# Performance work log

Hardware: AMD Instinct MI355X
Metric: run time of the kernel (lower is better)

Reference implementation:

```python
import jax, jax.numpy as jnp
import numpy as np

B, S = 4096, 4096
NS, FDIM = 16, 64


def _ln(x, g, b):
    mu = jnp.mean(x, axis=-1, keepdims=True)
    v = jnp.mean((x - mu) ** 2, axis=-1, keepdims=True)
    return (x - mu) / jnp.sqrt(v + 1e-5) * g + b


def _rolling_vol_mean(returns, w):
    # mean over all length-w windows of unbiased std (matches per-window torch.std loop)
    Bn, L = returns.shape
    z = jnp.zeros((Bn, 1), returns.dtype)
    c1 = jnp.concatenate([z, jnp.cumsum(returns, axis=1)], axis=1)
    c2 = jnp.concatenate([z, jnp.cumsum(returns * returns, axis=1)], axis=1)
    s = c1[:, w:] - c1[:, :-w]    # [B, L-w+1] window sums
    s2 = c2[:, w:] - c2[:, :-w]
    var = (s2 - s * s / w) / (w - 1)
    return jnp.mean(jnp.sqrt(jnp.maximum(var, 0.0)), axis=1, keepdims=True)


def setup_inputs() -> dict:
    key = jax.random.key(0)
    ks = jax.random.split(key, 24)
    r = lambda i, shp: jax.random.normal(ks[i], shp, jnp.float32) * 0.05
    return {
        'price_series': jax.random.uniform(ks[0], (B, S, 1), jnp.float32) * 10.0 + 1.0,
        're_W': r(1, (4, 4, 64)), 're_b': r(2, (4, 64)),
        're_g': jnp.ones((4, 64), jnp.float32), 're_beta': jnp.zeros((4, 64), jnp.float32),
        'rh_W1': r(3, (256, 64)), 'rh_b1': r(4, (64,)), 'rh_W2': r(5, (64, 4)), 'rh_b2': r(6, (4,)),
        'rv_W': r(7, (3, 128)), 'rv_b': r(8, (128,)),
        'rv_g': jnp.ones((128,), jnp.float32), 'rv_beta': jnp.zeros((128,), jnp.float32),
        'vs_W': r(9, (128, 128)), 'vs_b': r(10, (128,)),
        'vs_g': jnp.ones((128,), jnp.float32), 'vs_beta': jnp.zeros((128,), jnp.float32),
        'vc_W1': r(11, (256, 64)), 'vc_b1': r(12, (64,)), 'vc_W2': r(13, (64, 4)), 'vc_b2': r(14, (4,)),
        'emb': r(15, (NS, FDIM)),
        'cn_W1': r(16, (576, 128)), 'cn_b1': r(17, (128,)),
        'cn_W2': r(18, (128, 64)), 'cn_b2': r(19, (64,)),
        'cn_W3': r(20, (64, 1)), 'cn_b3': r(21, (1,)),
    }


def reference(price_series, re_W, re_b, re_g, re_beta, rh_W1, rh_b1, rh_W2, rh_b2,
              rv_W, rv_b, rv_g, rv_beta, vs_W, vs_b, vs_g, vs_beta,
              vc_W1, vc_b1, vc_W2, vc_b2, emb, cn_W1, cn_b1, cn_W2, cn_b2, cn_W3, cn_b3):
    prices = price_series[:, :, 0]            # [B,S]
    Bn, Sn = prices.shape
    # --- MarketRegimeEncoder: SMA-20 via prefix sums (the per-step torch loop) ---
    cs = jnp.cumsum(prices, axis=1)
    shifted = jnp.concatenate([jnp.zeros((Bn, 20), prices.dtype), cs[:, :-20]], axis=1)
    counts = jnp.minimum(jnp.arange(Sn) + 1, 20).astype(prices.dtype)
    sma20 = (cs - shifted) / counts           # (sma_5 is computed but unused in original)
    trend = jnp.mean((prices - sma20) / (sma20 + 1e-8), axis=1, keepdims=True)
    p10 = prices[:, Sn - 10:Sn - 9]
    momentum = (prices[:, -1:] - p10) / (p10 + 1e-8)
    pmean = jnp.mean(prices, axis=1, keepdims=True)
    mean_rev = (prices[:, -1:] - pmean) / (pmean + 1e-8)
    pstd = jnp.std(prices, axis=1, keepdims=True, ddof=1)
    cycle = pstd / (pmean + 1e-8)
    combined = jnp.concatenate([trend, momentum, mean_rev, cycle], axis=1)  # [B,4]
    h = jax.nn.relu(jnp.einsum('bi,kio->bko', combined, re_W) + re_b[None])  # [B,4,64]
    h = _ln(h, re_g[None], re_beta[None])
    regime_features = h.reshape(Bn, -1)        # [B,256] (trend|momentum|mean_rev|cycle)
    logits = jax.nn.relu(regime_features @ rh_W1 + rh_b1) @ rh_W2 + rh_b2
    regime_probs = jax.nn.softmax(logits, axis=1)
    # --- VolatilityEncodingModule ---
    logp = jnp.log(jnp.maximum(price_series, 1e-8))
    returns = jnp.diff(logp, axis=1)[:, :, 0]  # [B,S-1]
    vol_in = jnp.concatenate([_rolling_vol_mean(returns, w) for w in (5, 10, 20)], axis=1)  # [B,3]
    rv = _ln(jax.nn.relu(vol_in @ rv_W + rv_b), rv_g, rv_beta)
    vs = _ln(jax.nn.relu(rv @ vs_W + vs_b), vs_g, vs_beta)
    vol_features = jnp.concatenate([rv, vs], axis=1)  # [B,256]
    vlogits = jax.nn.relu(vol_features @ vc_W1 + vc_b1) @ vc_W2 + vc_b2
    vol_regime = jax.nn.softmax(vlogits, axis=1)
    # --- OptionsStrategyEncoder: vectorized over strategies ---
    mv = jnp.concatenate([regime_features, vol_features], axis=1)  # [B,512]
    mvp = mv @ cn_W1[:512]                    # [B,128]
    ep = emb @ cn_W1[512:]                    # [NS,128]
    h1 = jax.nn.relu(mvp[:, None, :] + ep[None, :, :] + cn_b1)  # [B,NS,128]
    h2 = jax.nn.relu(h1 @ cn_W2 + cn_b2)      # [B,NS,64]
    scores = (h2 @ cn_W3 + cn_b3)[:, :, 0]    # [B,NS]
    return regime_features, regime_probs, vol_features, vol_regime, scores
```

## Files before the change

kernel.cpp:

```cpp
#include <hip/hip_runtime.h>
#include <math.h>

#define NROWS 4096
#define SLEN  4096
#define RETN  4095
#define CHK   20

__global__ __launch_bounds__(256) void k_ep(const float* __restrict__ emb,
                                            const float* __restrict__ cn_W1,
                                            const float* __restrict__ cn_b1,
                                            float* __restrict__ ep) {
    int idx = blockIdx.x * 256 + threadIdx.x;
    if (idx >= 16 * 128) return;
    int n = idx >> 7, o = idx & 127;
    float acc = cn_b1[o];
    const float* w = cn_W1 + 512 * 128;
    for (int i = 0; i < 64; ++i) acc = fmaf(emb[n * 64 + i], w[i * 128 + o], acc);
    ep[idx] = acc;
}

__global__ void k_stats(const float* __restrict__ price,
                        float* __restrict__ combined,
                        float* __restrict__ volin) {
    __shared__ float scm[260 * CHK];
    __shared__ float red[6][4];

    const int tid = threadIdx.x;
    const int row = blockIdx.x;
    const float* pr = price + (size_t)row * SLEN;

    float pA = 0.f, pB = 0.f;
    if (tid == 0) { pA = pr[SLEN - 10]; pB = pr[SLEN - 1]; }

    if (tid < 40) { scm[tid] = 0.f; scm[258 * CHK + tid] = 0.f; }

    #pragma unroll
    for (int it = 0; it < 4; ++it) {
        const int i = it * 256 + tid;
        const float4 v = ((const float4*)pr)[i];
        *(float4*)&scm[(2 + (i >> 2)) * CHK + ((4 * i) & 15)] = v;
    }
    __syncthreads();

    const int s0 = tid * 16;

    float hb[20], x_[16];
    *(float4*)&hb[0] = *(const float4*)&scm[tid * CHK + 12];
    #pragma unroll
    for (int k = 0; k < 4; ++k)
        *(float4*)&hb[4 + 4 * k] = *(const float4*)&scm[(tid + 1) * CHK + 4 * k];
    #pragma unroll
    for (int k = 0; k < 4; ++k)
        *(float4*)&x_[4 * k] = *(const float4*)&scm[(tid + 2) * CHK + 4 * k];
    const float pn = scm[(tid + 3) * CHK];

    float W = 0.f;
    #pragma unroll
    for (int k = 0; k < 20; ++k) W += hb[k];
    float st = 0.f, s1p = 0.f, s2p = 0.f;
    #pragma unroll
    for (int d = 0; d < 16; ++d) {
        const float x = x_[d];
        W += x - hb[d];
        float inv_cnt = 0.05f;
        if (s0 == 0)                 inv_cnt = 1.0f / (float)(d + 1);
        else if (s0 == 16 && d < 3)  inv_cnt = 1.0f / (float)(17 + d);
        const float sma = W * inv_cnt;
        st  = fmaf(x - sma, __builtin_amdgcn_rcpf(sma + 1e-8f), st);
        s1p += x;
        s2p = fmaf(x, x, s2p);
    }

    float lg[17];
    #pragma unroll
    for (int d = 0; d < 16; ++d) lg[d] = __builtin_amdgcn_logf(fmaxf(x_[d], 1e-8f));
    lg[16] = __builtin_amdgcn_logf(fmaxf(pn, 1e-8f));
    float rs[36];
    #pragma unroll
    for (int d = 0; d < 16; ++d) rs[d] = lg[d + 1] - lg[d];

    __syncthreads();
    #pragma unroll
    for (int k = 0; k < 4; ++k)
        *(float4*)&scm[(tid + 2) * CHK + 4 * k] = *(const float4*)&rs[4 * k];
    __syncthreads();

    #pragma unroll
    for (int k = 0; k < 4; ++k)
        *(float4*)&rs[16 + 4 * k] = *(const float4*)&scm[(tid + 3) * CHK + 4 * k];
    *(float4*)&rs[32] = *(const float4*)&scm[(tid + 4) * CHK];

    float S5 = 0.f, Q5 = 0.f, S10 = 0.f, Q10 = 0.f, S20 = 0.f, Q20 = 0.f;
    #pragma unroll
    for (int j = 0; j < 20; ++j) {
        const float x = rs[j];
        S20 += x; Q20 = fmaf(x, x, Q20);
        if (j < 10) { S10 += x; Q10 = fmaf(x, x, Q10); }
        if (j < 5)  { S5  += x; Q5  = fmaf(x, x, Q5); }
    }

    #define SQT(S, Q, invw) \
        __builtin_amdgcn_sqrtf(fmaxf(fmaf(-(S) * (invw), (S), (Q)), 0.f))

    float v5 = 0.f, v10 = 0.f, v20 = 0.f;
    if (tid < 254) {
        #pragma unroll
        for (int d = 0; d < 16; ++d) {
            v5  += SQT(S5,  Q5,  0.2f);
            v10 += SQT(S10, Q10, 0.1f);
            v20 += SQT(S20, Q20, 0.05f);
            const float xo = rs[d], qo = xo * xo;
            const float a5 = rs[d + 5], a10 = rs[d + 10], a20 = rs[d + 20];
            S5  += a5  - xo;  Q5  = fmaf(a5,  a5,  Q5)  - qo;
            S10 += a10 - xo;  Q10 = fmaf(a10, a10, Q10) - qo;
            S20 += a20 - xo;  Q20 = fmaf(a20, a20, Q20) - qo;
        }
    } else {
        #pragma unroll
        for (int d = 0; d < 16; ++d) {
            const int i = s0 + d;
            if (i < 4091) v5  += SQT(S5,  Q5,  0.2f);
            if (i < 4086) v10 += SQT(S10, Q10, 0.1f);
            if (i < 4076) v20 += SQT(S20, Q20, 0.05f);
            const float xo = rs[d], qo = xo * xo;
            const float a5 = rs[d + 5], a10 = rs[d + 10], a20 = rs[d + 20];
            S5  += a5  - xo;  Q5  = fmaf(a5,  a5,  Q5)  - qo;
            S10 += a10 - xo;  Q10 = fmaf(a10, a10, Q10) - qo;
            S20 += a20 - xo;  Q20 = fmaf(a20, a20, Q20) - qo;
        }
    }
    #undef SQT

    {
        float vals[6] = {s1p, s2p, st, v5, v10, v20};
        const int lane = tid & 63, wid = tid >> 6;
        #pragma unroll
        for (int v = 0; v < 6; ++v) {
            float x = vals[v];
            for (int o = 32; o > 0; o >>= 1) x += __shfl_xor(x, o, 64);
            if (lane == 0) red[v][wid] = x;
        }
    }
    __syncthreads();
    if (tid == 0) {
        const float sum_p  = red[0][0] + red[0][1] + red[0][2] + red[0][3];
        const float sum_p2 = red[1][0] + red[1][1] + red[1][2] + red[1][3];
        const float sum_t  = red[2][0] + red[2][1] + red[2][2] + red[2][3];
        const float sv5    = red[3][0] + red[3][1] + red[3][2] + red[3][3];
        const float sv10   = red[4][0] + red[4][1] + red[4][2] + red[4][3];
        const float sv20   = red[5][0] + red[5][1] + red[5][2] + red[5][3];
        const float pmean = sum_p * (1.f / 4096.f);
        const float varp  = fmaf(-sum_p * (1.f / 4096.f), sum_p, sum_p2) * (1.f / 4095.f);
        const float pstd  = __builtin_amdgcn_sqrtf(fmaxf(varp, 0.f));
        const float ipm   = __builtin_amdgcn_rcpf(pmean + 1e-8f);
        combined[row * 4 + 0] = sum_t * (1.f / 4096.f);
        combined[row * 4 + 1] = (pB - pA) * __builtin_amdgcn_rcpf(pA + 1e-8f);
        combined[row * 4 + 2] = (pB - pmean) * ipm;
        combined[row * 4 + 3] = pstd * ipm;
        const float LN2 = 0.6931471805599453f;
        volin[row * 3 + 0] = sv5  * (LN2 * 0.5f                 / 4091.f);
        volin[row * 3 + 1] = sv10 * (LN2 * (1.f / 3.f)          / 4086.f);
        volin[row * 3 + 2] = sv20 * (LN2 * 0.22941573387056174f / 4076.f);
    }
}

__global__ __launch_bounds__(512, 2) void k_mc(const float* __restrict__ combined,
                                               const float* __restrict__ volin,
                                               const float* __restrict__ re_W,  const float* __restrict__ re_b,
                                               const float* __restrict__ re_g,  const float* __restrict__ re_be,
                                               const float* __restrict__ rh_W1, const float* __restrict__ rh_b1,
                                               const float* __restrict__ rh_W2, const float* __restrict__ rh_b2,
                                               const float* __restrict__ rv_W,  const float* __restrict__ rv_b,
                                               const float* __restrict__ rv_g,  const float* __restrict__ rv_be,
                                               const float* __restrict__ vs_W,  const float* __restrict__ vs_b,
                                               const float* __restrict__ vs_g,  const float* __restrict__ vs_be,
                                               const float* __restrict__ vc_W1, const float* __restrict__ vc_b1,
                                               const float* __restrict__ vc_W2, const float* __restrict__ vc_b2,
                                               const float* __restrict__ cn_W1,
                                               const float* __restrict__ cn_W2,
                                               const float* __restrict__ cn_b2,
                                               const float* __restrict__ cn_W3,
                                               const float* __restrict__ cn_b3,
                                               const float* __restrict__ ep,
                                               float* __restrict__ out_rf, float* __restrict__ out_rp,
                                               float* __restrict__ out_vf, float* __restrict__ out_vr,
                                               float* __restrict__ scores) {
    __shared__ __align__(16) float w2s[128 * 64];
    __shared__ __align__(16) float epb[16][132];
    __shared__ __align__(16) float rf_lds[8][256];
    __shared__ __align__(16) float vf_lds[8][256];
    __shared__ __align__(16) float psx[4][8][128];
    __shared__ __align__(16) float mvp_s[8][132];
    __shared__ float hid_s[8][64];
    __shared__ float prt[8][4];
    __shared__ float cmb_s[8][4];
    __shared__ float vol_s[8][3];

    const int tid  = threadIdx.x;
    const int lane = tid & 63;
    const int wid  = tid >> 6;
    const int row0 = blockIdx.x * 8;

    #pragma unroll
    for (int k = 0; k < 4; ++k) {
        const int idx = k * 512 + tid;
        *(float4*)&w2s[4 * idx] = *(const float4*)(cn_W2 + 4 * idx);
    }
    {
        const int ns = tid >> 5, c4 = (tid & 31) * 4;
        *(float4*)&epb[ns][c4] = *(const float4*)(ep + ns * 128 + c4);
    }
    if (tid < 32) cmb_s[tid >> 2][tid & 3] = combined[(size_t)(row0 + (tid >> 2)) * 4 + (tid & 3)];
    else if (tid < 56) { int t = tid - 32; vol_s[t / 3][t % 3] = volin[(size_t)(row0 + t / 3) * 3 + t % 3]; }
    __syncthreads();

    const int role = wid & 3;
    const int rg   = (wid >> 2) * 4;

    {
        const float* w = re_W + role * 256;
        const float w0 = w[lane], w1 = w[64 + lane], w2 = w[128 + lane], w3 = w[192 + lane];
        const float b  = re_b[role * 64 + lane];
        const float gg = re_g[role * 64 + lane], bb = re_be[role * 64 + lane];
        float h[4], sm[4], sq[4];
        #pragma unroll
        for (int r = 0; r < 4; ++r) {
            const int rr = rg + r;
            float v = fmaf(cmb_s[rr][0], w0, fmaf(cmb_s[rr][1], w1,
                      fmaf(cmb_s[rr][2], w2, fmaf(cmb_s[rr][3], w3, b))));
            h[r] = fmaxf(v, 0.f);
            sm[r] = h[r]; sq[r] = h[r] * h[r];
        }
        #pragma unroll
        for (int off = 32; off > 0; off >>= 1) {
            #pragma unroll
            for (int r = 0; r < 4; ++r) {
                sm[r] += __shfl_xor(sm[r], off, 64);
                sq[r] += __shfl_xor(sq[r], off, 64);
            }
        }
        #pragma unroll
        for (int r = 0; r < 4; ++r) {
            const float mu  = sm[r] * (1.f / 64.f);
            const float var = fmaxf(sq[r] * (1.f / 64.f) - mu * mu, 0.f);
            const float y = (h[r] - mu) * rsqrtf(var + 1e-5f) * gg + bb;
            rf_lds[rg + r][role * 64 + lane] = y;
            out_rf[(size_t)(row0 + rg + r) * 256 + role * 64 + lane] = y;
        }
    }
    __syncthreads();

    {
        const int i0 = role * 64;
        float acc[4] = {0.f, 0.f, 0.f, 0.f};
        for (int i = 0; i < 64; ++i) {
            const float wv = rh_W1[(size_t)(i0 + i) * 64 + lane];
            #pragma unroll
            for (int r = 0; r < 4; ++r) acc[r] = fmaf(rf_lds[rg + r][i0 + i], wv, acc[r]);
        }
        #pragma unroll
        for (int r = 0; r < 4; ++r) psx[role][rg + r][lane] = acc[r];
    }
    __syncthreads();

    {
        const int r = tid >> 6, o = tid & 63;
        const float v = psx[0][r][o] + psx[1][r][o] + psx[2][r][o] + psx[3][r][o] + rh_b1[o];
        hid_s[r][o] = fmaxf(v, 0.f);
    }
    __syncthreads();

    if (tid < 32) {
        const int r = tid >> 2, j = tid & 3;
        float acc = rh_b2[j];
        for (int i = 0; i < 64; ++i) acc = fmaf(hid_s[r][i], rh_W2[i * 4 + j], acc);
        float m = acc;
        m = fmaxf(m, __shfl_xor(m, 1, 64));
        m = fmaxf(m, __shfl_xor(m, 2, 64));
        const float e = expf(acc - m);
        float s = e;
        s += __shfl_xor(s, 1, 64);
        s += __shfl_xor(s, 2, 64);
        out_rp[(size_t)(row0 + r) * 4 + j] = e / s;
    }

    {
        const int o = tid & 127, g = tid >> 7;
        const float w0 = rv_W[o], w1 = rv_W[128 + o], w2 = rv_W[256 + o];
        const float b = rv_b[o], gg = rv_g[o], bb = rv_be[o];
        float h[2], sm[2], sq[2];
        #pragma unroll
        for (int r2 = 0; r2 < 2; ++r2) {
            const int r = g * 2 + r2;
            float v = fmaf(vol_s[r][0], w0, fmaf(vol_s[r][1], w1, fmaf(vol_s[r][2], w2, b)));
            h[r2] = fmaxf(v, 0.f);
            sm[r2] = h[r2]; sq[r2] = h[r2] * h[r2];
        }
        #pragma unroll
        for (int off = 32; off > 0; off >>= 1) {
            #pragma unroll
            for (int r2 = 0; r2 < 2; ++r2) {
                sm[r2] += __shfl_xor(sm[r2], off, 64);
                sq[r2] += __shfl_xor(sq[r2], off, 64);
            }
        }
        if (lane == 0) {
            #pragma unroll
            for (int r2 = 0; r2 < 2; ++r2) { prt[wid][r2 * 2] = sm[r2]; prt[wid][r2 * 2 + 1] = sq[r2]; }
        }
        __syncthreads();
        #pragma unroll
        for (int r2 = 0; r2 < 2; ++r2) {
            const float S = prt[2 * g][2 * r2]     + prt[2 * g + 1][2 * r2];
            const float Q = prt[2 * g][2 * r2 + 1] + prt[2 * g + 1][2 * r2 + 1];
            const float mu  = S * (1.f / 128.f);
            const float var = fmaxf(Q * (1.f / 128.f) - mu * mu, 0.f);
            const float y = (h[r2] - mu) * rsqrtf(var + 1e-5f) * gg + bb;
            vf_lds[g * 2 + r2][o] = y;
            out_vf[(size_t)(row0 + g * 2 + r2) * 256 + o] = y;
        }
    }
    __syncthreads();

    {
        const int o = tid & 127, g = tid >> 7;
        float acc[2];
        const float b = vs_b[o];
        acc[0] = b; acc[1] = b;
        for (int i = 0; i < 128; ++i) {
            const float wv = vs_W[(size_t)i * 128 + o];
            #pragma unroll
            for (int r2 = 0; r2 < 2; ++r2) acc[r2] = fmaf(vf_lds[g * 2 + r2][i], wv, acc[r2]);
        }
        const float gg = vs_g[o], bb = vs_be[o];
        float h[2], sm[2], sq[2];
        #pragma unroll
        for (int r2 = 0; r2 < 2; ++r2) {
            h[r2] = fmaxf(acc[r2], 0.f);
            sm[r2] = h[r2]; sq[r2] = h[r2] * h[r2];
        }
        #pragma unroll
        for (int off = 32; off > 0; off >>= 1) {
            #pragma unroll
            for (int r2 = 0; r2 < 2; ++r2) {
                sm[r2] += __shfl_xor(sm[r2], off, 64);
                sq[r2] += __shfl_xor(sq[r2], off, 64);
            }
        }
        __syncthreads();
        if (lane == 0) {
            #pragma unroll
            for (int r2 = 0; r2 < 2; ++r2) { prt[wid][r2 * 2] = sm[r2]; prt[wid][r2 * 2 + 1] = sq[r2]; }
        }
        __syncthreads();
        #pragma unroll
        for (int r2 = 0; r2 < 2; ++r2) {
            const float S = prt[2 * g][2 * r2]     + prt[2 * g + 1][2 * r2];
            const float Q = prt[2 * g][2 * r2 + 1] + prt[2 * g + 1][2 * r2 + 1];
            const float mu  = S * (1.f / 128.f);
            const float var = fmaxf(Q * (1.f / 128.f) - mu * mu, 0.f);
            const float y = (h[r2] - mu) * rsqrtf(var + 1e-5f) * gg + bb;
            vf_lds[g * 2 + r2][128 + o] = y;
            out_vf[(size_t)(row0 + g * 2 + r2) * 256 + 128 + o] = y;
        }
    }
    __syncthreads();

    {
        const int i0 = role * 64;
        float acc[4] = {0.f, 0.f, 0.f, 0.f};
        for (int i = 0; i < 64; ++i) {
            const float wv = vc_W1[(size_t)(i0 + i) * 64 + lane];
            #pragma unroll
            for (int r = 0; r < 4; ++r) acc[r] = fmaf(vf_lds[rg + r][i0 + i], wv, acc[r]);
        }
        #pragma unroll
        for (int r = 0; r < 4; ++r) psx[role][rg + r][lane] = acc[r];
    }
    __syncthreads();

    {
        const int r = tid >> 6, o = tid & 63;
        const float v = psx[0][r][o] + psx[1][r][o] + psx[2][r][o] + psx[3][r][o] + vc_b1[o];
        hid_s[r][o] = fmaxf(v, 0.f);
    }
    __syncthreads();
    if (tid < 32) {
        const int r = tid >> 2, j = tid & 3;
        float acc = vc_b2[j];
        for (int i = 0; i < 64; ++i) acc = fmaf(hid_s[r][i], vc_W2[i * 4 + j], acc);
        float m = acc;
        m = fmaxf(m, __shfl_xor(m, 1, 64));
        m = fmaxf(m, __shfl_xor(m, 2, 64));
        const float e = expf(acc - m);
        float s = e;
        s += __shfl_xor(s, 1, 64);
        s += __shfl_xor(s, 2, 64);
        out_vr[(size_t)(row0 + r) * 4 + j] = e / s;
    }
    __syncthreads();

    {
        const int p = lane >> 5;
        const int q = lane & 31;
        const float* mbase = (role < 2) ? &rf_lds[0][0] + role * 128
                                        : &vf_lds[0][0] + (role - 2) * 128;
        float acc[4][4] = {{0.f}};
        #pragma unroll 8
        for (int s = 0; s < 64; ++s) {
            const int i = 2 * s + p;
            const float4 w1v = *(const float4*)(cn_W1 + (size_t)(role * 128 + i) * 128 + 4 * q);
            #pragma unroll
            for (int r = 0; r < 4; ++r) {
                const float m = mbase[(rg + r) * 256 + i];
                acc[r][0] = fmaf(m, w1v.x, acc[r][0]);
                acc[r][1] = fmaf(m, w1v.y, acc[r][1]);
                acc[r][2] = fmaf(m, w1v.z, acc[r][2]);
                acc[r][3] = fmaf(m, w1v.w, acc[r][3]);
            }
        }
        #pragma unroll
        for (int r = 0; r < 4; ++r) {
            #pragma unroll
            for (int k = 0; k < 4; ++k) acc[r][k] += __shfl_xor(acc[r][k], 32, 64);
        }
        if (p == 0) {
            #pragma unroll
            for (int r = 0; r < 4; ++r)
                *(float4*)&psx[role][rg + r][4 * q] =
                    make_float4(acc[r][0], acc[r][1], acc[r][2], acc[r][3]);
        }
    }
    __syncthreads();

    #pragma unroll
    for (int k = 0; k < 2; ++k) {
        const int idx = k * 512 + tid;
        const int r = idx >> 7, c = idx & 127;
        mvp_s[r][c] = psx[0][r][c] + psx[1][r][c] + psx[2][r][c] + psx[3][r][c];
    }
    __syncthreads();

    {
        const int rgB = tid >> 8;
        const int nst = tid & 255;
        const int ns  = nst >> 4;
        const int t   = nst & 15;
        float acc[4][4];
        #pragma unroll
        for (int r = 0; r < 4; ++r)
            #pragma unroll
            for (int k = 0; k < 4; ++k) acc[r][k] = 0.f;

        #pragma unroll 2
        for (int c = 0; c < 128; c += 4) {
            float4 m4[4];
            #pragma unroll
            for (int r = 0; r < 4; ++r) m4[r] = *(const float4*)&mvp_s[rgB * 4 + r][c];
            const float4 e4 = *(const float4*)&epb[ns][c];
            {   const float4 w2v = *(const float4*)&w2s[(c + 0) * 64 + 4 * t];
                #pragma unroll
                for (int r = 0; r < 4; ++r) {
                    const float h = fmaxf(m4[r].x + e4.x, 0.f);
                    acc[r][0] = fmaf(h, w2v.x, acc[r][0]); acc[r][1] = fmaf(h, w2v.y, acc[r][1]);
                    acc[r][2] = fmaf(h, w2v.z, acc[r][2]); acc[r][3] = fmaf(h, w2v.w, acc[r][3]); } }
            {   const float4 w2v = *(const float4*)&w2s[(c + 1) * 64 + 4 * t];
                #pragma unroll
                for (int r = 0; r < 4; ++r) {
                    const float h = fmaxf(m4[r].y + e4.y, 0.f);
                    acc[r][0] = fmaf(h, w2v.x, acc[r][0]); acc[r][1] = fmaf(h, w2v.y, acc[r][1]);
                    acc[r][2] = fmaf(h, w2v.z, acc[r][2]); acc[r][3] = fmaf(h, w2v.w, acc[r][3]); } }
            {   const float4 w2v = *(const float4*)&w2s[(c + 2) * 64 + 4 * t];
                #pragma unroll
                for (int r = 0; r < 4; ++r) {
                    const float h = fmaxf(m4[r].z + e4.z, 0.f);
                    acc[r][0] = fmaf(h, w2v.x, acc[r][0]); acc[r][1] = fmaf(h, w2v.y, acc[r][1]);
                    acc[r][2] = fmaf(h, w2v.z, acc[r][2]); acc[r][3] = fmaf(h, w2v.w, acc[r][3]); } }
            {   const float4 w2v = *(const float4*)&w2s[(c + 3) * 64 + 4 * t];
                #pragma unroll
                for (int r = 0; r < 4; ++r) {
                    const float h = fmaxf(m4[r].w + e4.w, 0.f);
                    acc[r][0] = fmaf(h, w2v.x, acc[r][0]); acc[r][1] = fmaf(h, w2v.y, acc[r][1]);
                    acc[r][2] = fmaf(h, w2v.z, acc[r][2]); acc[r][3] = fmaf(h, w2v.w, acc[r][3]); } }
        }

        const float4 b2v = *(const float4*)(cn_b2 + 4 * t);
        const float4 w3v = *(const float4*)(cn_W3 + 4 * t);
        const float  b3v = cn_b3[0];
        #pragma unroll
        for (int r = 0; r < 4; ++r) {
            float s =      fmaxf(acc[r][0] + b2v.x, 0.f) * w3v.x;
            s = fmaf(fmaxf(acc[r][1] + b2v.y, 0.f), w3v.y, s);
            s = fmaf(fmaxf(acc[r][2] + b2v.z, 0.f), w3v.z, s);
            s = fmaf(fmaxf(acc[r][3] + b2v.w, 0.f), w3v.w, s);
            s += __shfl_xor(s, 1, 64);
            s += __shfl_xor(s, 2, 64);
            s += __shfl_xor(s, 4, 64);
            s += __shfl_xor(s, 8, 64);
            if (t == 0) scores[(size_t)(row0 + rgB * 4 + r) * 16 + ns] = s + b3v;
        }
    }
}

extern "C" void kernel_launch(void* const* d_in, const int* in_sizes, int n_in,
                              void* d_out, int out_size, void* d_ws, size_t ws_size,
                              hipStream_t stream) {
    (void)in_sizes; (void)n_in; (void)out_size; (void)ws_size;

    const float* price = (const float*)d_in[0];
    const float* re_W  = (const float*)d_in[1];
    const float* re_b  = (const float*)d_in[2];
    const float* re_g  = (const float*)d_in[3];
    const float* re_be = (const float*)d_in[4];
    const float* rh_W1 = (const float*)d_in[5];
    const float* rh_b1 = (const float*)d_in[6];
    const float* rh_W2 = (const float*)d_in[7];
    const float* rh_b2 = (const float*)d_in[8];
    const float* rv_W  = (const float*)d_in[9];
    const float* rv_b  = (const float*)d_in[10];
    const float* rv_g  = (const float*)d_in[11];
    const float* rv_be = (const float*)d_in[12];
    const float* vs_W  = (const float*)d_in[13];
    const float* vs_b  = (const float*)d_in[14];
    const float* vs_g  = (const float*)d_in[15];
    const float* vs_be = (const float*)d_in[16];
    const float* vc_W1 = (const float*)d_in[17];
    const float* vc_b1 = (const float*)d_in[18];
    const float* vc_W2 = (const float*)d_in[19];
    const float* vc_b2 = (const float*)d_in[20];
    const float* emb   = (const float*)d_in[21];
    const float* cn_W1 = (const float*)d_in[22];
    const float* cn_b1 = (const float*)d_in[23];
    const float* cn_W2 = (const float*)d_in[24];
    const float* cn_b2 = (const float*)d_in[25];
    const float* cn_W3 = (const float*)d_in[26];
    const float* cn_b3 = (const float*)d_in[27];

    float* out    = (float*)d_out;
    float* out_rf = out;
    float* out_rp = out_rf + 4096 * 256;
    float* out_vf = out_rp + 4096 * 4;
    float* out_vr = out_vf + 4096 * 256;
    float* out_sc = out_vr + 4096 * 4;

    float* ws       = (float*)d_ws;
    float* combined = ws;
    float* volin    = combined + 4096 * 4;
    float* ep       = volin + 4096 * 3;

    hipLaunchKernelGGL(k_ep,    dim3(8),    dim3(256), 0, stream, emb, cn_W1, cn_b1, ep);
    hipLaunchKernelGGL(k_stats, dim3(4096), dim3(256), 0, stream, price, combined, volin);
    hipLaunchKernelGGL(k_mc,    dim3(512),  dim3(512), 0, stream, combined, volin,
                       re_W, re_b, re_g, re_be, rh_W1, rh_b1, rh_W2, rh_b2,
                       rv_W, rv_b, rv_g, rv_be, vs_W, vs_b, vs_g, vs_be,
                       vc_W1, vc_b1, vc_W2, vc_b2,
                       cn_W1, cn_W2, cn_b2, cn_W3, cn_b3, ep,
                       out_rf, out_rp, out_vf, out_vr, out_sc);
}
```

Measured before the change: 110.3 us.

## Halve k_mc block to 4 rows/256 threads and alias LDS scratch buffers

```diff
diff --git a/kernel.cpp b/kernel.cpp
--- a/kernel.cpp
+++ b/kernel.cpp
@@ -19,9 +19,9 @@
     ep[idx] = acc;
 }
 
-__global__ void k_stats(const float* __restrict__ price,
-                        float* __restrict__ combined,
-                        float* __restrict__ volin) {
+__global__ __launch_bounds__(256, 4) void k_stats(const float* __restrict__ price,
+                                                  float* __restrict__ combined,
+                                                  float* __restrict__ volin) {
     __shared__ float scm[260 * CHK];
     __shared__ float red[6][4];
 
@@ -164,7 +164,7 @@
     }
 }
 
-__global__ __launch_bounds__(512, 2) void k_mc(const float* __restrict__ combined,
+__global__ __launch_bounds__(256, 3) void k_mc(const float* __restrict__ combined,
                                                const float* __restrict__ volin,
                                                const float* __restrict__ re_W,  const float* __restrict__ re_b,
                                                const float* __restrict__ re_g,  const float* __restrict__ re_be,
@@ -186,48 +186,42 @@
                                                float* __restrict__ out_vf, float* __restrict__ out_vr,
                                                float* __restrict__ scores) {
     __shared__ __align__(16) float w2s[128 * 64];
-    __shared__ __align__(16) float epb[16][132];
-    __shared__ __align__(16) float rf_lds[8][256];
-    __shared__ __align__(16) float vf_lds[8][256];
-    __shared__ __align__(16) float psx[4][8][128];
-    __shared__ __align__(16) float mvp_s[8][132];
-    __shared__ float hid_s[8][64];
-    __shared__ float prt[8][4];
-    __shared__ float cmb_s[8][4];
-    __shared__ float vol_s[8][3];
+    __shared__ __align__(16) float uni[2112];
+    __shared__ __align__(16) float rf_lds[4][256];
+    __shared__ __align__(16) float vf_lds[4][256];
+    __shared__ __align__(16) float mvp_s[4][128];
+    __shared__ float hid_s[4][64];
+    __shared__ float prt[4][4];
+    __shared__ float cmb_s[4][4];
+    __shared__ float vol_s[4][3];
 
     const int tid  = threadIdx.x;
     const int lane = tid & 63;
     const int wid  = tid >> 6;
-    const int row0 = blockIdx.x * 8;
-
-    #pragma unroll
-    for (int k = 0; k < 4; ++k) {
-        const int idx = k * 512 + tid;
+    const int row0 = blockIdx.x * 4;
+
+    const float4 ep0 = ((const float4*)ep)[2 * tid];
+    const float4 ep1 = ((const float4*)ep)[2 * tid + 1];
+
+    #pragma unroll
+    for (int k = 0; k < 8; ++k) {
+        const int idx = k * 256 + tid;
         *(float4*)&w2s[4 * idx] = *(const float4*)(cn_W2 + 4 * idx);
     }
-    {
-        const int ns = tid >> 5, c4 = (tid & 31) * 4;
-        *(float4*)&epb[ns][c4] = *(const float4*)(ep + ns * 128 + c4);
-    }
-    if (tid < 32) cmb_s[tid >> 2][tid & 3] = combined[(size_t)(row0 + (tid >> 2)) * 4 + (tid & 3)];
-    else if (tid < 56) { int t = tid - 32; vol_s[t / 3][t % 3] = volin[(size_t)(row0 + t / 3) * 3 + t % 3]; }
-    __syncthreads();
-
-    const int role = wid & 3;
-    const int rg   = (wid >> 2) * 4;
-
-    {
-        const float* w = re_W + role * 256;
+    if (tid < 16) cmb_s[tid >> 2][tid & 3] = combined[(size_t)(row0 + (tid >> 2)) * 4 + (tid & 3)];
+    else if (tid < 28) { int t = tid - 16; vol_s[t / 3][t % 3] = volin[(size_t)(row0 + t / 3) * 3 + t % 3]; }
+    __syncthreads();
+
+    {
+        const float* w = re_W + wid * 256;
         const float w0 = w[lane], w1 = w[64 + lane], w2 = w[128 + lane], w3 = w[192 + lane];
-        const float b  = re_b[role * 64 + lane];
-        const float gg = re_g[role * 64 + lane], bb = re_be[role * 64 + lane];
+        const float b  = re_b[wid * 64 + lane];
+        const float gg = re_g[wid * 64 + lane], bb = re_be[wid * 64 + lane];
         float h[4], sm[4], sq[4];
         #pragma unroll
         for (int r = 0; r < 4; ++r) {
-            const int rr = rg + r;
-            float v = fmaf(cmb_s[rr][0], w0, fmaf(cmb_s[rr][1], w1,
-                      fmaf(cmb_s[rr][2], w2, fmaf(cmb_s[rr][3], w3, b))));
+            float v = fmaf(cmb_s[r][0], w0, fmaf(cmb_s[r][1], w1,
+                      fmaf(cmb_s[r][2], w2, fmaf(cmb_s[r][3], w3, b))));
             h[r] = fmaxf(v, 0.f);
             sm[r] = h[r]; sq[r] = h[r] * h[r];
         }
@@ -244,33 +238,34 @@
             const float mu  = sm[r] * (1.f / 64.f);
             const float var = fmaxf(sq[r] * (1.f / 64.f) - mu * mu, 0.f);
             const float y = (h[r] - mu) * rsqrtf(var + 1e-5f) * gg + bb;
-            rf_lds[rg + r][role * 64 + lane] = y;
-            out_rf[(size_t)(row0 + rg + r) * 256 + role * 64 + lane] = y;
-        }
-    }
-    __syncthreads();
-
-    {
-        const int i0 = role * 64;
+            rf_lds[r][wid * 64 + lane] = y;
+            out_rf[(size_t)(row0 + r) * 256 + wid * 64 + lane] = y;
+        }
+    }
+    __syncthreads();
+
+    {
+        const int i0 = wid * 64;
         float acc[4] = {0.f, 0.f, 0.f, 0.f};
         for (int i = 0; i < 64; ++i) {
             const float wv = rh_W1[(size_t)(i0 + i) * 64 + lane];
             #pragma unroll
-            for (int r = 0; r < 4; ++r) acc[r] = fmaf(rf_lds[rg + r][i0 + i], wv, acc[r]);
-        }
-        #pragma unroll
-        for (int r = 0; r < 4; ++r) psx[role][rg + r][lane] = acc[r];
+            for (int r = 0; r < 4; ++r) acc[r] = fmaf(rf_lds[r][i0 + i], wv, acc[r]);
+        }
+        #pragma unroll
+        for (int r = 0; r < 4; ++r) uni[wid * 512 + r * 128 + lane] = acc[r];
     }
     __syncthreads();
 
     {
         const int r = tid >> 6, o = tid & 63;
-        const float v = psx[0][r][o] + psx[1][r][o] + psx[2][r][o] + psx[3][r][o] + rh_b1[o];
+        const float v = uni[r * 128 + o] + uni[512 + r * 128 + o]
+                      + uni[1024 + r * 128 + o] + uni[1536 + r * 128 + o] + rh_b1[o];
         hid_s[r][o] = fmaxf(v, 0.f);
     }
     __syncthreads();
 
-    if (tid < 32) {
+    if (tid < 16) {
         const int r = tid >> 2, j = tid & 3;
         float acc = rh_b2[j];
         for (int i = 0; i < 64; ++i) acc = fmaf(hid_s[r][i], rh_W2[i * 4 + j], acc);
@@ -367,25 +362,26 @@
     __syncthreads();
 
     {
-        const int i0 = role * 64;
+        const int i0 = wid * 64;
         float acc[4] = {0.f, 0.f, 0.f, 0.f};
         for (int i = 0; i < 64; ++i) {
             const float wv = vc_W1[(size_t)(i0 + i) * 64 + lane];
             #pragma unroll
-            for (int r = 0; r < 4; ++r) acc[r] = fmaf(vf_lds[rg + r][i0 + i], wv, acc[r]);
-        }
-        #pragma unroll
-        for (int r = 0; r < 4; ++r) psx[role][rg + r][lane] = acc[r];
+            for (int r = 0; r < 4; ++r) acc[r] = fmaf(vf_lds[r][i0 + i], wv, acc[r]);
+        }
+        #pragma unroll
+        for (int r = 0; r < 4; ++r) uni[wid * 512 + r * 128 + lane] = acc[r];
     }
     __syncthreads();
 
     {
         const int r = tid >> 6, o = tid & 63;
-        const float v = psx[0][r][o] + psx[1][r][o] + psx[2][r][o] + psx[3][r][o] + vc_b1[o];
+        const float v = uni[r * 128 + o] + uni[512 + r * 128 + o]
+                      + uni[1024 + r * 128 + o] + uni[1536 + r * 128 + o] + vc_b1[o];
         hid_s[r][o] = fmaxf(v, 0.f);
     }
     __syncthreads();
-    if (tid < 32) {
+    if (tid < 16) {
         const int r = tid >> 2, j = tid & 3;
         float acc = vc_b2[j];
         for (int i = 0; i < 64; ++i) acc = fmaf(hid_s[r][i], vc_W2[i * 4 + j], acc);
@@ -403,16 +399,16 @@
     {
         const int p = lane >> 5;
         const int q = lane & 31;
-        const float* mbase = (role < 2) ? &rf_lds[0][0] + role * 128
-                                        : &vf_lds[0][0] + (role - 2) * 128;
+        const float* mbase = (wid < 2) ? &rf_lds[0][0] + wid * 128
+                                       : &vf_lds[0][0] + (wid - 2) * 128;
         float acc[4][4] = {{0.f}};
         #pragma unroll 8
         for (int s = 0; s < 64; ++s) {
             const int i = 2 * s + p;
-            const float4 w1v = *(const float4*)(cn_W1 + (size_t)(role * 128 + i) * 128 + 4 * q);
+            const float4 w1v = *(const float4*)(cn_W1 + (size_t)(wid * 128 + i) * 128 + 4 * q);
             #pragma unroll
             for (int r = 0; r < 4; ++r) {
-                const float m = mbase[(rg + r) * 256 + i];
+                const float m = mbase[r * 256 + i];
                 acc[r][0] = fmaf(m, w1v.x, acc[r][0]);
                 acc[r][1] = fmaf(m, w1v.y, acc[r][1]);
                 acc[r][2] = fmaf(m, w1v.z, acc[r][2]);
@@ -427,7 +423,7 @@
         if (p == 0) {
             #pragma unroll
             for (int r = 0; r < 4; ++r)
-                *(float4*)&psx[role][rg + r][4 * q] =
+                *(float4*)&uni[wid * 512 + r * 128 + 4 * q] =
                     make_float4(acc[r][0], acc[r][1], acc[r][2], acc[r][3]);
         }
     }
@@ -435,17 +431,23 @@
 
     #pragma unroll
     for (int k = 0; k < 2; ++k) {
-        const int idx = k * 512 + tid;
+        const int idx = k * 256 + tid;
         const int r = idx >> 7, c = idx & 127;
-        mvp_s[r][c] = psx[0][r][c] + psx[1][r][c] + psx[2][r][c] + psx[3][r][c];
-    }
-    __syncthreads();
-
-    {
-        const int rgB = tid >> 8;
-        const int nst = tid & 255;
-        const int ns  = nst >> 4;
-        const int t   = nst & 15;
+        mvp_s[r][c] = uni[r * 128 + c] + uni[512 + r * 128 + c]
+                    + uni[1024 + r * 128 + c] + uni[1536 + r * 128 + c];
+    }
+    __syncthreads();
+
+    {
+        const int ns = tid >> 4, c = (tid * 8) & 127;
+        *(float4*)&uni[ns * 132 + c]     = ep0;
+        *(float4*)&uni[ns * 132 + c + 4] = ep1;
+    }
+    __syncthreads();
+
+    {
+        const int ns = tid >> 4;
+        const int t  = tid & 15;
         float acc[4][4];
         #pragma unroll
         for (int r = 0; r < 4; ++r)
@@ -456,8 +458,8 @@
         for (int c = 0; c < 128; c += 4) {
             float4 m4[4];
             #pragma unroll
-            for (int r = 0; r < 4; ++r) m4[r] = *(const float4*)&mvp_s[rgB * 4 + r][c];
-            const float4 e4 = *(const float4*)&epb[ns][c];
+            for (int r = 0; r < 4; ++r) m4[r] = *(const float4*)&mvp_s[r][c];
+            const float4 e4 = *(const float4*)&uni[ns * 132 + c];
             {   const float4 w2v = *(const float4*)&w2s[(c + 0) * 64 + 4 * t];
                 #pragma unroll
                 for (int r = 0; r < 4; ++r) {
@@ -497,7 +499,7 @@
             s += __shfl_xor(s, 2, 64);
             s += __shfl_xor(s, 4, 64);
             s += __shfl_xor(s, 8, 64);
-            if (t == 0) scores[(size_t)(row0 + rgB * 4 + r) * 16 + ns] = s + b3v;
+            if (t == 0) scores[(size_t)(row0 + r) * 16 + ns] = s + b3v;
         }
     }
 }
@@ -550,7 +552,7 @@
 
     hipLaunchKernelGGL(k_ep,    dim3(8),    dim3(256), 0, stream, emb, cn_W1, cn_b1, ep);
     hipLaunchKernelGGL(k_stats, dim3(4096), dim3(256), 0, stream, price, combined, volin);
-    hipLaunchKernelGGL(k_mc,    dim3(512),  dim3(512), 0, stream, combined, volin,
+    hipLaunchKernelGGL(k_mc,    dim3(1024), dim3(256), 0, stream, combined, volin,
                        re_W, re_b, re_g, re_be, rh_W1, rh_b1, rh_W2, rh_b2,
                        rv_W, rv_b, rv_g, rv_be, vs_W, vs_b, vs_g, vs_be,
                        vc_W1, vc_b1, vc_W2, vc_b2,
```

New measurement: 163.1 us. 1.48x slower.
